# Kernel tuning notes

Hardware: AMD Instinct MI355X
Metric: run time of the kernel (lower is better)

## Reference

```python
import jax, jax.numpy as jnp
import numpy as np

B, T, D = 2, 2048, 4096
H, KVH = 32, 8            # query heads, kv heads (GQA)
HD = D // H               # 128
N_REP = H // KVH          # 4
ROPE_THETA = 500000.0


def _rope_freqs(seq_len, head_dim, theta):
    inv = 1.0 / (theta ** (np.arange(0, head_dim, 2, dtype=np.float32) / head_dim))
    ang = np.outer(np.arange(seq_len, dtype=np.float32), inv)  # [T, HD/2]
    return jnp.asarray(np.cos(ang)), jnp.asarray(np.sin(ang))


def setup_inputs() -> dict:
    key = jax.random.key(0)
    ks = jax.random.split(key, 5)
    scale = 1.0 / np.sqrt(D)
    x = jax.random.normal(ks[0], (B, T, D), dtype=jnp.float32) * 0.05
    wq = jax.random.normal(ks[1], (H * HD, D), dtype=jnp.float32) * scale
    wk = jax.random.normal(ks[2], (KVH * HD, D), dtype=jnp.float32) * scale
    wv = jax.random.normal(ks[3], (KVH * HD, D), dtype=jnp.float32) * scale
    wo = jax.random.normal(ks[4], (D, H * HD), dtype=jnp.float32) * scale
    fc, fs = _rope_freqs(T, HD, ROPE_THETA)
    return {"x": x, "wq": wq, "wk": wk, "wv": wv, "wo": wo,
            "freqs_cos": fc, "freqs_sin": fs, "start_pos": 0}


def _apply_rope(t, cos, sin):
    # t: [B, T, h, HD]; cos/sin: [T, HD/2] -> broadcast [1, T, 1, HD/2]
    b, s, h, hd = t.shape
    tr = t.reshape(b, s, h, hd // 2, 2)
    te, to = tr[..., 0], tr[..., 1]
    c = cos[None, :, None, :]
    s_ = sin[None, :, None, :]
    out = jnp.stack([te * c - to * s_, te * s_ + to * c], axis=-1)
    return out.reshape(b, s, h, hd)


def reference(x, wq, wk, wv, wo, freqs_cos, freqs_sin, start_pos):
    # Projections (F.linear convention: y = x @ W.T)
    q = jnp.einsum('btd,od->bto', x, wq).reshape(B, T, H, HD)
    k = jnp.einsum('btd,od->bto', x, wk).reshape(B, T, KVH, HD)
    v = jnp.einsum('btd,od->bto', x, wv).reshape(B, T, KVH, HD)
    # RoPE on q and k
    q = _apply_rope(q, freqs_cos, freqs_sin)
    k = _apply_rope(k, freqs_cos, freqs_sin)
    # prefill at start_pos=0: cache[:T] == k, v; repeat kv heads for GQA
    keys = jnp.repeat(k, N_REP, axis=2)    # [B, T, H, HD]
    values = jnp.repeat(v, N_REP, axis=2)  # [B, T, H, HD]
    scale = 1.0 / jnp.sqrt(jnp.float32(HD))
    # NOTE: the source module accepts a mask but never applies it -> unmasked softmax
    scores = jnp.einsum('bthd,bshd->bhts', q, keys) * scale  # [B, H, T, T]
    probs = jax.nn.softmax(scores, axis=-1)
    ctx = jnp.einsum('bhts,bshd->bthd', probs, values)       # [B, T, H, HD]
    ctx = ctx.reshape(B, T, H * HD)
    return jnp.einsum('bte,oe->bto', ctx, wo)
```

## Files before the change

### kernel.cpp

```cpp
#include <hip/hip_runtime.h>

#define B_ 2
#define T_ 2048
#define D_ 4096
#define H_ 32
#define KVH_ 8
#define HD_ 128

typedef float f32x4 __attribute__((ext_vector_type(4)));
typedef float f32x2 __attribute__((ext_vector_type(2)));
typedef unsigned int u32x4 __attribute__((ext_vector_type(4)));
typedef unsigned short u16x4 __attribute__((ext_vector_type(4)));
typedef unsigned short u16x2 __attribute__((ext_vector_type(2)));
typedef __bf16 bf16x8 __attribute__((ext_vector_type(8)));

__device__ __forceinline__ unsigned short f2bf(float f) {
  union { float f; unsigned int u; } x; x.f = f;
  unsigned int r = x.u + 0x7fffu + ((x.u >> 16) & 1u);
  return (unsigned short)(r >> 16);
}

__device__ __forceinline__ bf16x8 ldb8(const unsigned short* p) {
  return __builtin_bit_cast(bf16x8, *(const u32x4*)p);
}

__device__ __forceinline__ f32x4 mfma16(bf16x8 a, bf16x8 b, f32x4 c) {
  return __builtin_amdgcn_mfma_f32_16x16x32_bf16(a, b, c, 0, 0, 0);
}

__device__ __forceinline__ void gl_lds16(const void* g, void* l) {
  __builtin_amdgcn_global_load_lds(
      (const __attribute__((address_space(1))) unsigned int*)g,
      (__attribute__((address_space(3))) unsigned int*)l, 16, 0, 0);
}

__global__ __launch_bounds__(256) void cast_bf16(const float* __restrict__ src,
                                                 unsigned short* __restrict__ dst, int n4) {
  int i = blockIdx.x * 256 + threadIdx.x;
  if (i >= n4) return;
  f32x4 v = *(const f32x4*)(src + (size_t)i * 4);
  u16x4 o; o.x = f2bf(v.x); o.y = f2bf(v.y); o.z = f2bf(v.z); o.w = f2bf(v.w);
  *(u16x4*)(dst + (size_t)i * 4) = o;
}

__global__ __launch_bounds__(256) void gemm_bt(const unsigned short* __restrict__ A,
                                               const unsigned short* __restrict__ Bt,
                                               float* __restrict__ C, int N) {
  const int m0 = blockIdx.y * 128, n0 = blockIdx.x * 128;
  const int tid = threadIdx.x, lane = tid & 63, wave = tid >> 6;
  const int quad = lane >> 4, l16 = lane & 15;
  const int wy = wave >> 1, wx = wave & 1;
  const int sw = l16 & 7;
  __shared__ unsigned short As[128 * 64];
  __shared__ unsigned short Bs[128 * 64];
  f32x4 acc[4][4];
#pragma unroll
  for (int i = 0; i < 4; ++i)
#pragma unroll
    for (int j = 0; j < 4; ++j) { f32x4 z = {0.f, 0.f, 0.f, 0.f}; acc[i][j] = z; }

  for (int k0 = 0; k0 < 4096; k0 += 64) {
#pragma unroll
    for (int p = 0; p < 4; ++p) {
      int c = p * 256 + tid;
      int row = c >> 3, gc = (c & 7) ^ (row & 7);
      gl_lds16(&A[(size_t)(m0 + row) * 4096 + k0 + gc * 8], &As[c * 8]);
    }
#pragma unroll
    for (int p = 0; p < 4; ++p) {
      int c = p * 256 + tid;
      int row = c >> 3, gc = (c & 7) ^ (row & 7);
      gl_lds16(&Bt[(size_t)(n0 + row) * 4096 + k0 + gc * 8], &Bs[c * 8]);
    }
    __syncthreads();
#pragma unroll
    for (int ks = 0; ks < 2; ++ks) {
      const int cp = ((ks * 4 + quad) ^ sw) * 8;
      bf16x8 af[4], bfr[4];
#pragma unroll
      for (int mt = 0; mt < 4; ++mt) af[mt] = ldb8(&As[(wy * 64 + mt * 16 + l16) * 64 + cp]);
#pragma unroll
      for (int nt = 0; nt < 4; ++nt) bfr[nt] = ldb8(&Bs[(wx * 64 + nt * 16 + l16) * 64 + cp]);
#pragma unroll
      for (int mt = 0; mt < 4; ++mt)
#pragma unroll
        for (int nt = 0; nt < 4; ++nt)
          acc[mt][nt] = mfma16(af[mt], bfr[nt], acc[mt][nt]);
    }
    __syncthreads();
  }
#pragma unroll
  for (int mt = 0; mt < 4; ++mt)
#pragma unroll
    for (int nt = 0; nt < 4; ++nt)
#pragma unroll
      for (int r = 0; r < 4; ++r) {
        int m = m0 + wy * 64 + mt * 16 + quad * 4 + r;
        int n = n0 + wx * 64 + nt * 16 + l16;
        C[(size_t)m * N + n] = acc[mt][nt][r];
      }
}

__global__ __launch_bounds__(256) void rope_q(const float* __restrict__ q,
                                              const float* __restrict__ fc,
                                              const float* __restrict__ fs,
                                              unsigned short* __restrict__ Qb) {
  int p = blockIdx.x * 256 + threadIdx.x;
  int i = p & 63;
  int h = (p >> 6) & 31;
  int t = (p >> 11) & 2047;
  int b = p >> 22;
  f32x2 v = *(const f32x2*)&q[(size_t)p * 2];
  float c = fc[t * 64 + i], s = fs[t * 64 + i];
  const float qs = 0.08838834764831845f;
  float e = (v.x * c - v.y * s) * qs;
  float od = (v.x * s + v.y * c) * qs;
  u16x2 w; w.x = f2bf(e); w.y = f2bf(od);
  *(u16x2*)&Qb[((size_t)(b * H_ + h) * T_ + t) * HD_ + 2 * i] = w;
}

__global__ __launch_bounds__(256) void rope_k(const float* __restrict__ k,
                                              const float* __restrict__ fc,
                                              const float* __restrict__ fs,
                                              unsigned short* __restrict__ Kb) {
  int p = blockIdx.x * 256 + threadIdx.x;
  int i = p & 63;
  int kvh = (p >> 6) & 7;
  int t = (p >> 9) & 2047;
  int b = p >> 20;
  f32x2 v = *(const f32x2*)&k[(size_t)p * 2];
  float c = fc[t * 64 + i], s = fs[t * 64 + i];
  float e = v.x * c - v.y * s;
  float od = v.x * s + v.y * c;
  u16x2 w; w.x = f2bf(e); w.y = f2bf(od);
  *(u16x2*)&Kb[((size_t)(b * KVH_ + kvh) * T_ + t) * HD_ + 2 * i] = w;
}

__global__ __launch_bounds__(256) void transpose_v(const float* __restrict__ v,
                                                   unsigned short* __restrict__ vt) {
  __shared__ unsigned short tile[64 * 72];
  const int hd0 = blockIdx.x * 64;
  const int t0 = blockIdx.y * 64;
  const int bk = blockIdx.z;
  const int b = bk >> 3, kvh = bk & 7;
  const int tid = threadIdx.x;
#pragma unroll
  for (int p = 0; p < 4; ++p) {
    int idx = tid + p * 256;
    int tl = idx >> 4, c4 = (idx & 15) << 2;
    f32x4 val = *(const f32x4*)&v[((size_t)(b * T_ + t0 + tl) * KVH_ + kvh) * HD_ + hd0 + c4];
#pragma unroll
    for (int j = 0; j < 4; ++j) tile[(c4 + j) * 72 + tl] = f2bf(val[j]);
  }
  __syncthreads();
#pragma unroll
  for (int p = 0; p < 2; ++p) {
    int idx = tid + p * 256;
    int hdl = idx >> 3, c8 = (idx & 7) << 3;
    *(u32x4*)&vt[((size_t)bk * HD_ + hd0 + hdl) * T_ + t0 + c8] = *(const u32x4*)&tile[hdl * 72 + c8];
  }
}

__global__ __launch_bounds__(256, 3) void attn(const unsigned short* __restrict__ Q,
                                               const unsigned short* __restrict__ K,
                                               const unsigned short* __restrict__ Vt,
                                               unsigned short* __restrict__ ctx) {
  const int qb = blockIdx.x;
  const int bh = blockIdx.y;
  const int b = bh >> 5, h = bh & 31;
  const int kvh = h >> 2;
  const unsigned short* Qh = Q + (size_t)(b * H_ + h) * T_ * HD_;
  const unsigned short* Kh = K + (size_t)(b * KVH_ + kvh) * T_ * HD_;
  const unsigned short* Vh = Vt + (size_t)(b * KVH_ + kvh) * HD_ * T_;
  const int tid = threadIdx.x, lane = tid & 63, wave = tid >> 6;
  const int quad = lane >> 4, l16 = lane & 15;
  const int sw = l16 & 7;
  __shared__ unsigned short Ks[64 * 128];
  __shared__ unsigned short Vs[128 * 64];
  __shared__ unsigned short Ps[4][32 * 72];

  const int q0 = qb * 128 + wave * 32;
  bf16x8 qf[2][4];
#pragma unroll
  for (int mt = 0; mt < 2; ++mt)
#pragma unroll
    for (int ks = 0; ks < 4; ++ks)
      qf[mt][ks] = ldb8(&Qh[(size_t)(q0 + mt * 16 + l16) * HD_ + ks * 32 + quad * 8]);

  f32x4 o[2][8];
#pragma unroll
  for (int mt = 0; mt < 2; ++mt)
#pragma unroll
    for (int f = 0; f < 8; ++f) { f32x4 z = {0.f, 0.f, 0.f, 0.f}; o[mt][f] = z; }
  float l_part[2][4] = {{0.f, 0.f, 0.f, 0.f}, {0.f, 0.f, 0.f, 0.f}};

  for (int kb = 0; kb < T_ / 64; ++kb) {
#pragma unroll
    for (int p = 0; p < 4; ++p) {
      int c = p * 256 + tid;
      int row = c >> 4, gc = (c & 15) ^ (row & 7);
      gl_lds16(&Kh[(size_t)(kb * 64 + row) * HD_ + gc * 8], &Ks[c * 8]);
    }
#pragma unroll
    for (int p = 0; p < 4; ++p) {
      int c = p * 256 + tid;
      int row = c >> 3, gc = (c & 7) ^ (row & 7);
      gl_lds16(&Vh[(size_t)row * T_ + kb * 64 + gc * 8], &Vs[c * 8]);
    }
    __syncthreads();

    f32x4 s[2][4];
#pragma unroll
    for (int mt = 0; mt < 2; ++mt)
#pragma unroll
      for (int nt = 0; nt < 4; ++nt) { f32x4 z = {0.f, 0.f, 0.f, 0.f}; s[mt][nt] = z; }
#pragma unroll
    for (int ks = 0; ks < 4; ++ks) {
      const int cp = ((ks * 4 + quad) ^ sw) * 8;
#pragma unroll
      for (int nt = 0; nt < 4; ++nt) {
        bf16x8 kf = ldb8(&Ks[(nt * 16 + l16) * 128 + cp]);
        s[0][nt] = mfma16(qf[0][ks], kf, s[0][nt]);
        s[1][nt] = mfma16(qf[1][ks], kf, s[1][nt]);
      }
    }

#pragma unroll
    for (int mt = 0; mt < 2; ++mt)
#pragma unroll
      for (int nt = 0; nt < 4; ++nt)
#pragma unroll
        for (int r = 0; r < 4; ++r) {
          float p_ = __expf(s[mt][nt][r]);
          l_part[mt][r] += p_;
          Ps[wave][(mt * 16 + quad * 4 + r) * 72 + nt * 16 + l16] = f2bf(p_);
        }

#pragma unroll
    for (int ks2 = 0; ks2 < 2; ++ks2) {
      const int cp = ((ks2 * 4 + quad) ^ sw) * 8;
      bf16x8 pf0 = ldb8(&Ps[wave][(l16) * 72 + ks2 * 32 + quad * 8]);
      bf16x8 pf1 = ldb8(&Ps[wave][(16 + l16) * 72 + ks2 * 32 + quad * 8]);
#pragma unroll
      for (int f = 0; f < 8; ++f) {
        bf16x8 vfr = ldb8(&Vs[(f * 16 + l16) * 64 + cp]);
        o[0][f] = mfma16(pf0, vfr, o[0][f]);
        o[1][f] = mfma16(pf1, vfr, o[1][f]);
      }
    }
    __syncthreads();
  }

  float rl[2][4];
#pragma unroll
  for (int mt = 0; mt < 2; ++mt)
#pragma unroll
    for (int r = 0; r < 4; ++r) {
      float l = l_part[mt][r];
      l += __shfl_xor(l, 1);
      l += __shfl_xor(l, 2);
      l += __shfl_xor(l, 4);
      l += __shfl_xor(l, 8);
      rl[mt][r] = 1.0f / l;
    }

#pragma unroll
  for (int mt = 0; mt < 2; ++mt)
#pragma unroll
    for (int f = 0; f < 8; ++f)
#pragma unroll
      for (int r = 0; r < 4; ++r) {
        int t = qb * 128 + wave * 32 + mt * 16 + quad * 4 + r;
        int hd = f * 16 + l16;
        ctx[((size_t)(b * T_ + t)) * D_ + h * HD_ + hd] = f2bf(o[mt][f][r] * rl[mt][r]);
      }
}

extern "C" void kernel_launch(void* const* d_in, const int* in_sizes, int n_in,
                              void* d_out, int out_size, void* d_ws, size_t ws_size,
                              hipStream_t stream) {
  const float* x  = (const float*)d_in[0];
  const float* wq = (const float*)d_in[1];
  const float* wk = (const float*)d_in[2];
  const float* wv = (const float*)d_in[3];
  const float* wo = (const float*)d_in[4];
  const float* fc = (const float*)d_in[5];
  const float* fs = (const float*)d_in[6];

  char* ws = (char*)d_ws;
  unsigned short* xb   = (unsigned short*)(ws + 0);
  unsigned short* wqb  = (unsigned short*)(ws + 33554432);
  unsigned short* wkb  = (unsigned short*)(ws + 67108864);
  unsigned short* wvb  = (unsigned short*)(ws + 75497472);
  unsigned short* wob  = (unsigned short*)(ws + 83886080);
  float*          kf   = (float*)(ws + 117440512);
  float*          vf   = (float*)(ws + 134217728);
  unsigned short* Qb   = (unsigned short*)(ws + 150994944);
  unsigned short* Kb   = (unsigned short*)(ws + 184549376);
  unsigned short* Vtb  = (unsigned short*)(ws + 192937984);
  unsigned short* ctxb = (unsigned short*)(ws + 117440512);
  float* qf  = (float*)d_out;
  float* out = (float*)d_out;

  cast_bf16<<<16384, 256, 0, stream>>>(x,  xb,  4194304);
  cast_bf16<<<16384, 256, 0, stream>>>(wq, wqb, 4194304);
  cast_bf16<<<4096,  256, 0, stream>>>(wk, wkb, 1048576);
  cast_bf16<<<4096,  256, 0, stream>>>(wv, wvb, 1048576);
  cast_bf16<<<16384, 256, 0, stream>>>(wo, wob, 4194304);

  gemm_bt<<<dim3(32, 32), 256, 0, stream>>>(xb, wqb, qf, 4096);
  gemm_bt<<<dim3(8, 32),  256, 0, stream>>>(xb, wkb, kf, 1024);
  gemm_bt<<<dim3(8, 32),  256, 0, stream>>>(xb, wvb, vf, 1024);

  rope_q<<<32768, 256, 0, stream>>>(qf, fc, fs, Qb);
  rope_k<<<8192,  256, 0, stream>>>(kf, fc, fs, Kb);
  transpose_v<<<dim3(2, 32, 16), 256, 0, stream>>>(vf, Vtb);

  attn<<<dim3(16, 64), 256, 0, stream>>>(Qb, Kb, Vtb, ctxb);

  gemm_bt<<<dim3(32, 32), 256, 0, stream>>>(ctxb, wob, out, 4096);
}
```

Baseline: 1.023 ms.

## Fuse RoPE and bf16 cast into projection GEMM epilogues, read K directly

Templates the GEMM epilogue so the Q and K projections apply RoPE (using a lane shuffle to fetch the pair element), scale, and write bf16 in head-major layout directly. The V projection now emits bf16, which the transpose reads instead of fp32. This removes the separate rope kernels and the fp32 round trips. The attention kernel also drops LDS staging of K, loading K fragments straight from global memory, and raises the occupancy hint from 3 to 4 blocks per CU. That trades LDS traffic and shared memory for uncoalesced global loads.

Result: slower. 1.468 ms (+43.5%).

```diff
diff --git a/kernel.cpp b/kernel.cpp
--- a/kernel.cpp
+++ b/kernel.cpp
@@ -43,9 +43,13 @@
   *(u16x4*)(dst + (size_t)i * 4) = o;
 }
 
+template <int EPI>
 __global__ __launch_bounds__(256) void gemm_bt(const unsigned short* __restrict__ A,
                                                const unsigned short* __restrict__ Bt,
-                                               float* __restrict__ C, int N) {
+                                               float* __restrict__ Cf,
+                                               unsigned short* __restrict__ C16,
+                                               const float* __restrict__ fc,
+                                               const float* __restrict__ fs, int N) {
   const int m0 = blockIdx.y * 128, n0 = blockIdx.x * 128;
   const int tid = threadIdx.x, lane = tid & 63, wave = tid >> 6;
   const int quad = lane >> 4, l16 = lane & 15;
@@ -89,6 +93,7 @@
     }
     __syncthreads();
   }
+
 #pragma unroll
   for (int mt = 0; mt < 4; ++mt)
 #pragma unroll
@@ -97,46 +102,29 @@
       for (int r = 0; r < 4; ++r) {
         int m = m0 + wy * 64 + mt * 16 + quad * 4 + r;
         int n = n0 + wx * 64 + nt * 16 + l16;
-        C[(size_t)m * N + n] = acc[mt][nt][r];
-      }
-}
-
-__global__ __launch_bounds__(256) void rope_q(const float* __restrict__ q,
-                                              const float* __restrict__ fc,
-                                              const float* __restrict__ fs,
-                                              unsigned short* __restrict__ Qb) {
-  int p = blockIdx.x * 256 + threadIdx.x;
-  int i = p & 63;
-  int h = (p >> 6) & 31;
-  int t = (p >> 11) & 2047;
-  int b = p >> 22;
-  f32x2 v = *(const f32x2*)&q[(size_t)p * 2];
-  float c = fc[t * 64 + i], s = fs[t * 64 + i];
-  const float qs = 0.08838834764831845f;
-  float e = (v.x * c - v.y * s) * qs;
-  float od = (v.x * s + v.y * c) * qs;
-  u16x2 w; w.x = f2bf(e); w.y = f2bf(od);
-  *(u16x2*)&Qb[((size_t)(b * H_ + h) * T_ + t) * HD_ + 2 * i] = w;
-}
-
-__global__ __launch_bounds__(256) void rope_k(const float* __restrict__ k,
-                                              const float* __restrict__ fc,
-                                              const float* __restrict__ fs,
-                                              unsigned short* __restrict__ Kb) {
-  int p = blockIdx.x * 256 + threadIdx.x;
-  int i = p & 63;
-  int kvh = (p >> 6) & 7;
-  int t = (p >> 9) & 2047;
-  int b = p >> 20;
-  f32x2 v = *(const f32x2*)&k[(size_t)p * 2];
-  float c = fc[t * 64 + i], s = fs[t * 64 + i];
-  float e = v.x * c - v.y * s;
-  float od = v.x * s + v.y * c;
-  u16x2 w; w.x = f2bf(e); w.y = f2bf(od);
-  *(u16x2*)&Kb[((size_t)(b * KVH_ + kvh) * T_ + t) * HD_ + 2 * i] = w;
-}
-
-__global__ __launch_bounds__(256) void transpose_v(const float* __restrict__ v,
+        float v = acc[mt][nt][r];
+        if constexpr (EPI == 0) {
+          Cf[(size_t)m * N + n] = v;
+        } else if constexpr (EPI == 3) {
+          C16[(size_t)m * N + n] = f2bf(v);
+        } else {
+          int b = m >> 11, t = m & 2047;
+          int hh = n >> 7, hd = n & 127;
+          float p = __shfl_xor(v, 1);
+          int fi = t * 64 + (hd >> 1);
+          float c = fc[fi], s = fs[fi];
+          float o = (hd & 1) ? (p * s + v * c) : (v * c - p * s);
+          if constexpr (EPI == 1) {
+            o *= 0.08838834764831845f;
+            C16[((size_t)(b * H_ + hh) * T_ + t) * HD_ + hd] = f2bf(o);
+          } else {
+            C16[((size_t)(b * KVH_ + hh) * T_ + t) * HD_ + hd] = f2bf(o);
+          }
+        }
+      }
+}
+
+__global__ __launch_bounds__(256) void transpose_v(const unsigned short* __restrict__ vb,
                                                    unsigned short* __restrict__ vt) {
   __shared__ unsigned short tile[64 * 72];
   const int hd0 = blockIdx.x * 64;
@@ -145,23 +133,24 @@
   const int b = bk >> 3, kvh = bk & 7;
   const int tid = threadIdx.x;
 #pragma unroll
-  for (int p = 0; p < 4; ++p) {
+  for (int p = 0; p < 2; ++p) {
     int idx = tid + p * 256;
-    int tl = idx >> 4, c4 = (idx & 15) << 2;
-    f32x4 val = *(const f32x4*)&v[((size_t)(b * T_ + t0 + tl) * KVH_ + kvh) * HD_ + hd0 + c4];
-#pragma unroll
-    for (int j = 0; j < 4; ++j) tile[(c4 + j) * 72 + tl] = f2bf(val[j]);
+    int tl = idx >> 3, c8 = (idx & 7) << 3;
+    u16x4 lo = *(const u16x4*)&vb[((size_t)(b * T_ + t0 + tl) * KVH_ + kvh) * HD_ + hd0 + c8];
+    u16x4 hi = *(const u16x4*)&vb[((size_t)(b * T_ + t0 + tl) * KVH_ + kvh) * HD_ + hd0 + c8 + 4];
+#pragma unroll
+    for (int j = 0; j < 4; ++j) { tile[(c8 + j) * 72 + tl] = lo[j]; tile[(c8 + 4 + j) * 72 + tl] = hi[j]; }
   }
   __syncthreads();
 #pragma unroll
   for (int p = 0; p < 2; ++p) {
     int idx = tid + p * 256;
     int hdl = idx >> 3, c8 = (idx & 7) << 3;
-    *(u32x4*)&vt[((size_t)bk * HD_ + hd0 + hdl) * T_ + t0 + c8] = *(const u32x4*)&tile[hdl * 72 + c8];
-  }
-}
-
-__global__ __launch_bounds__(256, 3) void attn(const unsigned short* __restrict__ Q,
+    *(u32x4*)&vt[((size_t)(bk * HD_ + hd0 + hdl)) * T_ + t0 + c8] = *(const u32x4*)&tile[hdl * 72 + c8];
+  }
+}
+
+__global__ __launch_bounds__(256, 4) void attn(const unsigned short* __restrict__ Q,
                                                const unsigned short* __restrict__ K,
                                                const unsigned short* __restrict__ Vt,
                                                unsigned short* __restrict__ ctx) {
@@ -175,7 +164,6 @@
   const int tid = threadIdx.x, lane = tid & 63, wave = tid >> 6;
   const int quad = lane >> 4, l16 = lane & 15;
   const int sw = l16 & 7;
-  __shared__ unsigned short Ks[64 * 128];
   __shared__ unsigned short Vs[128 * 64];
   __shared__ unsigned short Ps[4][32 * 72];
 
@@ -195,12 +183,6 @@
   float l_part[2][4] = {{0.f, 0.f, 0.f, 0.f}, {0.f, 0.f, 0.f, 0.f}};
 
   for (int kb = 0; kb < T_ / 64; ++kb) {
-#pragma unroll
-    for (int p = 0; p < 4; ++p) {
-      int c = p * 256 + tid;
-      int row = c >> 4, gc = (c & 15) ^ (row & 7);
-      gl_lds16(&Kh[(size_t)(kb * 64 + row) * HD_ + gc * 8], &Ks[c * 8]);
-    }
 #pragma unroll
     for (int p = 0; p < 4; ++p) {
       int c = p * 256 + tid;
@@ -216,10 +198,9 @@
       for (int nt = 0; nt < 4; ++nt) { f32x4 z = {0.f, 0.f, 0.f, 0.f}; s[mt][nt] = z; }
 #pragma unroll
     for (int ks = 0; ks < 4; ++ks) {
-      const int cp = ((ks * 4 + quad) ^ sw) * 8;
 #pragma unroll
       for (int nt = 0; nt < 4; ++nt) {
-        bf16x8 kf = ldb8(&Ks[(nt * 16 + l16) * 128 + cp]);
+        bf16x8 kf = ldb8(&Kh[(size_t)(kb * 64 + nt * 16 + l16) * HD_ + ks * 32 + quad * 8]);
         s[0][nt] = mfma16(qf[0][ks], kf, s[0][nt]);
         s[1][nt] = mfma16(qf[1][ks], kf, s[1][nt]);
       }
@@ -293,13 +274,11 @@
   unsigned short* wkb  = (unsigned short*)(ws + 67108864);
   unsigned short* wvb  = (unsigned short*)(ws + 75497472);
   unsigned short* wob  = (unsigned short*)(ws + 83886080);
-  float*          kf   = (float*)(ws + 117440512);
-  float*          vf   = (float*)(ws + 134217728);
+  unsigned short* ctxb = (unsigned short*)(ws + 117440512);
+  unsigned short* vb   = (unsigned short*)(ws + 134217728);
   unsigned short* Qb   = (unsigned short*)(ws + 150994944);
   unsigned short* Kb   = (unsigned short*)(ws + 184549376);
   unsigned short* Vtb  = (unsigned short*)(ws + 192937984);
-  unsigned short* ctxb = (unsigned short*)(ws + 117440512);
-  float* qf  = (float*)d_out;
   float* out = (float*)d_out;
 
   cast_bf16<<<16384, 256, 0, stream>>>(x,  xb,  4194304);
@@ -308,15 +287,13 @@
   cast_bf16<<<4096,  256, 0, stream>>>(wv, wvb, 1048576);
   cast_bf16<<<16384, 256, 0, stream>>>(wo, wob, 4194304);
 
-  gemm_bt<<<dim3(32, 32), 256, 0, stream>>>(xb, wqb, qf, 4096);
-  gemm_bt<<<dim3(8, 32),  256, 0, stream>>>(xb, wkb, kf, 1024);
-  gemm_bt<<<dim3(8, 32),  256, 0, stream>>>(xb, wvb, vf, 1024);
-
-  rope_q<<<32768, 256, 0, stream>>>(qf, fc, fs, Qb);
-  rope_k<<<8192,  256, 0, stream>>>(kf, fc, fs, Kb);
-  transpose_v<<<dim3(2, 32, 16), 256, 0, stream>>>(vf, Vtb);
+  gemm_bt<1><<<dim3(32, 32), 256, 0, stream>>>(xb, wqb, nullptr, Qb, fc, fs, 4096);
+  gemm_bt<2><<<dim3(8, 32),  256, 0, stream>>>(xb, wkb, nullptr, Kb, fc, fs, 1024);
+  gemm_bt<3><<<dim3(8, 32),  256, 0, stream>>>(xb, wvb, nullptr, vb, fc, fs, 1024);
+
+  transpose_v<<<dim3(2, 32, 16), 256, 0, stream>>>(vb, Vtb);
 
   attn<<<dim3(16, 64), 256, 0, stream>>>(Qb, Kb, Vtb, ctxb);
 
-  gemm_bt<<<dim3(32, 32), 256, 0, stream>>>(ctxb, wob, out, 4096);
-}
+  gemm_bt<0><<<dim3(32, 32), 256, 0, stream>>>(ctxb, wob, out, nullptr, fc, fs, 4096);
+}
```
